# Performance work log

Measured on AMD Instinct MI355X. Metric: run time of the kernel, lower is better.

Reference implementation:

```python
import jax, jax.numpy as jnp
import numpy as np

N_WIRES = 10
DIM = 1 << N_WIRES  # 1024
EPS = 1e-12

_CNOT = jnp.array([[1, 0, 0, 0],
                   [0, 1, 0, 0],
                   [0, 0, 0, 1],
                   [0, 0, 1, 0]], dtype=jnp.complex64)

# signs[i, j] = (-1)^{bit_j(i)} for single-Z Pauli string on wire j (qubit 0 = MSB)
_bits = (np.arange(DIM)[:, None] >> (N_WIRES - 1 - np.arange(N_WIRES))[None, :]) & 1
_Z_SIGNS = jnp.asarray(1.0 - 2.0 * _bits, dtype=jnp.float32)  # (DIM, N_WIRES)


def _rx_gate(theta):
    c = jnp.cos(theta / 2).astype(jnp.complex64)
    s = jnp.sin(theta / 2).astype(jnp.complex64)
    return jnp.stack([jnp.stack([c, -1j * s]), jnp.stack([-1j * s, c])])


def _ry_gate(theta):
    c = jnp.cos(theta / 2).astype(jnp.complex64)
    s = jnp.sin(theta / 2).astype(jnp.complex64)
    return jnp.stack([jnp.stack([c, -s]), jnp.stack([s, c])])


def _apply_1q(psi, gate, q):
    # psi: (N, DIM) complex64; apply 2x2 gate on qubit q (qubit 0 = MSB)
    N = psi.shape[0]
    left, right = 1 << q, 1 << (N_WIRES - 1 - q)
    psi = psi.reshape(N, left, 2, right)
    psi = jnp.einsum('ab,nxby->nxay', gate, psi)
    return psi.reshape(N, DIM)


def _apply_2q(psi, gate, q0, q1):
    # gate: (4,4) acting on qubits (q0, q1) in that order
    G = gate.reshape(2, 2, 2, 2)
    if q0 > q1:
        G = jnp.transpose(G, (1, 0, 3, 2))
        q0, q1 = q1, q0
    N = psi.shape[0]
    a = 1 << q0
    b = 1 << (q1 - q0 - 1)
    c = 1 << (N_WIRES - 1 - q1)
    psi = psi.reshape(N, a, 2, b, 2, c)
    psi = jnp.einsum('ijkl,nxkylz->nxiyjz', G, psi)
    return psi.reshape(N, DIM)


def setup_inputs() -> dict:
    key = jax.random.key(0)
    k1, k2, k3, k4 = jax.random.split(key, 4)
    x = jax.random.normal(k1, (4, 1024, DIM), dtype=jnp.float32)
    rx0 = jax.random.normal(k2, (N_WIRES,), dtype=jnp.float32)
    ry0 = jax.random.normal(k3, (N_WIRES,), dtype=jnp.float32)
    ry1 = jax.random.normal(k4, (N_WIRES,), dtype=jnp.float32)
    return {"x": x, "rx0": rx0, "ry0": ry0, "ry1": ry1}


def reference(x, rx0, ry0, ry1):
    B, T, C = x.shape
    x_flat = x.reshape(B * T, C)
    # amplitude encoding: L2-normalize each row into a complex state vector
    norm = jnp.linalg.norm(x_flat, axis=1, keepdims=True)
    psi = (x_flat / jnp.maximum(norm, EPS)).astype(jnp.complex64)  # (N, DIM)
    # layer 1: RX then RY on each wire
    for j in range(N_WIRES):
        psi = _apply_1q(psi, _rx_gate(rx0[j]), j)
        psi = _apply_1q(psi, _ry_gate(ry0[j]), j)
    # CNOT ring
    for j in range(N_WIRES):
        psi = _apply_2q(psi, _CNOT, j, (j + 1) % N_WIRES)
    # layer 2: RY on each wire
    for j in range(N_WIRES):
        psi = _apply_1q(psi, _ry_gate(ry1[j]), j)
    # expectation values of Z on each wire: sum_i |psi_i|^2 * (-1)^{bit_j(i)}
    probs = psi.real ** 2 + psi.imag ** 2  # (N, DIM) float32
    out = probs @ _Z_SIGNS                  # (N, N_WIRES)
    return out.reshape(B, T, N_WIRES).astype(jnp.float32)
```

## Files before the change

### kernel.cpp

```cpp
#include <hip/hip_runtime.h>

#define NW 10

__device__ __forceinline__ int gperm(int v) {
    #pragma unroll
    for (int k = 9; k >= 0; --k) {
        const int cs = 9 - k;
        const int ts = 9 - ((k + 1) % NW);
        v ^= ((v >> cs) & 1) << ts;
    }
    return v;
}

__device__ __forceinline__ int PF(int i) {
    return i + ((i >> 5) << 2) + ((i >> 8) << 3);
}
#define PBUF 1176

template<int SH>
__device__ __forceinline__ void cg(float* re, float* im,
                                   float ar, float ai, float br, float bi) {
    #pragma unroll
    for (int base = 0; base < 16; base += (2 << SH)) {
        #pragma unroll
        for (int off = 0; off < (1 << SH); ++off) {
            const int r0 = base + off, r1 = r0 + (1 << SH);
            const float v0r = re[r0], v0i = im[r0];
            const float v1r = re[r1], v1i = im[r1];
            re[r0] =  ar * v0r - ai * v0i + br * v1r - bi * v1i;
            im[r0] =  ar * v0i + ai * v0r + br * v1i + bi * v1r;
            re[r1] = -br * v0r - bi * v0i + ar * v1r + ai * v1i;
            im[r1] =  bi * v0r - br * v0i + ar * v1i - ai * v1r;
        }
    }
}

template<int SH>
__device__ __forceinline__ void rg(float* re, float* im, float c, float s) {
    #pragma unroll
    for (int base = 0; base < 16; base += (2 << SH)) {
        #pragma unroll
        for (int off = 0; off < (1 << SH); ++off) {
            const int r0 = base + off, r1 = r0 + (1 << SH);
            const float v0r = re[r0], v0i = im[r0];
            const float v1r = re[r1], v1i = im[r1];
            re[r0] = c * v0r - s * v1r;  im[r0] = c * v0i - s * v1i;
            re[r1] = s * v0r + c * v1r;  im[r1] = s * v0i + c * v1i;
        }
    }
}

__global__ __launch_bounds__(64) void qsa_main(
    const float* __restrict__ x,
    const float* __restrict__ rx0,
    const float* __restrict__ ry0,
    const float* __restrict__ ry1,
    float* __restrict__ out) {

    __shared__ __align__(16) float reb[PBUF];
    __shared__ __align__(16) float imb[PBUF];
    __shared__ float cf[64];

    const int t = threadIdx.x;
    const int n = blockIdx.x;

    if (t < NW) {
        float sx, cx, sy0, cy0, sy1, cy1;
        sincosf(0.5f * rx0[t], &sx,  &cx);
        sincosf(0.5f * ry0[t], &sy0, &cy0);
        sincosf(0.5f * ry1[t], &sy1, &cy1);
        cf[4 * t + 0] =  cy0 * cx;
        cf[4 * t + 1] =  sy0 * sx;
        cf[4 * t + 2] = -sy0 * cx;
        cf[4 * t + 3] = -cy0 * sx;
        cf[40 + 2 * t]     = cy1;
        cf[40 + 2 * t + 1] = sy1;
    }

    float re[16], im[16];
    const float* xr = x + ((size_t)n << 10) + (t << 4);
    float ss = 0.f;
    #pragma unroll
    for (int r = 0; r < 16; r += 4) {
        const float4 v = *reinterpret_cast<const float4*>(xr + r);
        re[r] = v.x; re[r + 1] = v.y; re[r + 2] = v.z; re[r + 3] = v.w;
        ss += v.x * v.x + v.y * v.y + v.z * v.z + v.w * v.w;
    }
    #pragma unroll
    for (int b = 32; b > 0; b >>= 1) ss += __shfl_xor(ss, b, 64);
    const float scale = 1.0f / fmaxf(sqrtf(ss), 1e-12f);

    __syncthreads();

    {
        const float ar = cf[36], ai = cf[37], br = cf[38], bi = cf[39];
        #pragma unroll
        for (int r = 0; r < 16; r += 2) {
            const float v0 = re[r] * scale, v1 = re[r + 1] * scale;
            re[r]     =  ar * v0 + br * v1;  im[r]     = ai * v0 + bi * v1;
            re[r + 1] = -br * v0 + ar * v1;  im[r + 1] = bi * v0 - ai * v1;
        }
    }
    cg<1>(re, im, cf[32], cf[33], cf[34], cf[35]);
    cg<2>(re, im, cf[28], cf[29], cf[30], cf[31]);
    cg<3>(re, im, cf[24], cf[25], cf[26], cf[27]);

    #pragma unroll
    for (int r = 0; r < 16; r += 4) {
        const int p = PF((t << 4) + r);
        *reinterpret_cast<float4*>(&reb[p]) = make_float4(re[r], re[r+1], re[r+2], re[r+3]);
        *reinterpret_cast<float4*>(&imb[p]) = make_float4(im[r], im[r+1], im[r+2], im[r+3]);
    }
    __syncthreads();
    {
        const int b0 = ((t >> 4) << 8) | (t & 15);
        #pragma unroll
        for (int r = 0; r < 16; ++r) {
            const int p = PF(b0 + (r << 4));
            re[r] = reb[p]; im[r] = imb[p];
        }
    }

    cg<0>(re, im, cf[20], cf[21], cf[22], cf[23]);
    cg<1>(re, im, cf[16], cf[17], cf[18], cf[19]);
    cg<2>(re, im, cf[12], cf[13], cf[14], cf[15]);
    cg<3>(re, im, cf[ 8], cf[ 9], cf[10], cf[11]);

    {
        const int b0 = ((t >> 4) << 8) | (t & 15);
        #pragma unroll
        for (int r = 0; r < 16; ++r) {
            const int p = PF(b0 + (r << 4));
            reb[p] = re[r]; imb[p] = im[r];
        }
    }
    __syncthreads();
    #pragma unroll
    for (int r = 0; r < 16; r += 4) {
        const int p = PF(((r >> 2) << 8) | (t << 2));
        float4 q = *reinterpret_cast<const float4*>(&reb[p]);
        re[r] = q.x; re[r+1] = q.y; re[r+2] = q.z; re[r+3] = q.w;
        q = *reinterpret_cast<const float4*>(&imb[p]);
        im[r] = q.x; im[r+1] = q.y; im[r+2] = q.z; im[r+3] = q.w;
    }

    cg<2>(re, im, cf[4], cf[5], cf[6], cf[7]);
    cg<3>(re, im, cf[0], cf[1], cf[2], cf[3]);

    #pragma unroll
    for (int r = 0; r < 16; r += 4) {
        const int p = PF(((r >> 2) << 8) | (t << 2));
        *reinterpret_cast<float4*>(&reb[p]) = make_float4(re[r], re[r+1], re[r+2], re[r+3]);
        *reinterpret_cast<float4*>(&imb[p]) = make_float4(im[r], im[r+1], im[r+2], im[r+3]);
    }
    __syncthreads();
    {
        const int gt = gperm(t << 4);
        #pragma unroll
        for (int r = 0; r < 16; ++r) {
            const int p = PF(gt ^ gperm(r));
            re[r] = reb[p]; im[r] = imb[p];
        }
    }

    rg<0>(re, im, cf[58], cf[59]);
    rg<1>(re, im, cf[56], cf[57]);
    rg<2>(re, im, cf[54], cf[55]);
    rg<3>(re, im, cf[52], cf[53]);

    #pragma unroll
    for (int r = 0; r < 16; r += 4) {
        const int p = PF((t << 4) + r);
        *reinterpret_cast<float4*>(&reb[p]) = make_float4(re[r], re[r+1], re[r+2], re[r+3]);
        *reinterpret_cast<float4*>(&imb[p]) = make_float4(im[r], im[r+1], im[r+2], im[r+3]);
    }
    __syncthreads();
    {
        const int b0 = ((t >> 4) << 8) | (t & 15);
        #pragma unroll
        for (int r = 0; r < 16; ++r) {
            const int p = PF(b0 + (r << 4));
            re[r] = reb[p]; im[r] = imb[p];
        }
    }

    rg<0>(re, im, cf[50], cf[51]);
    rg<1>(re, im, cf[48], cf[49]);
    rg<2>(re, im, cf[46], cf[47]);
    rg<3>(re, im, cf[44], cf[45]);

    {
        const int b0 = ((t >> 4) << 8) | (t & 15);
        #pragma unroll
        for (int r = 0; r < 16; ++r) {
            const int p = PF(b0 + (r << 4));
            reb[p] = re[r]; imb[p] = im[r];
        }
    }
    __syncthreads();
    #pragma unroll
    for (int r = 0; r < 16; r += 4) {
        const int p = PF(((r >> 2) << 8) | (t << 2));
        float4 q = *reinterpret_cast<const float4*>(&reb[p]);
        re[r] = q.x; re[r+1] = q.y; re[r+2] = q.z; re[r+3] = q.w;
        q = *reinterpret_cast<const float4*>(&imb[p]);
        im[r] = q.x; im[r+1] = q.y; im[r+2] = q.z; im[r+3] = q.w;
    }

    rg<2>(re, im, cf[42], cf[43]);
    rg<3>(re, im, cf[40], cf[41]);

    float P = 0.f, a0 = 0.f, a1 = 0.f, a8 = 0.f, a9 = 0.f;
    #pragma unroll
    for (int r = 0; r < 16; ++r) {
        const float p = re[r] * re[r] + im[r] * im[r];
        P  += p;
        a0 += (r & 8) ? -p : p;
        a1 += (r & 4) ? -p : p;
        a8 += (r & 2) ? -p : p;
        a9 += (r & 1) ? -p : p;
    }
    #pragma unroll
    for (int b = 1; b < 64; b <<= 1) {
        a0 += __shfl_xor(a0, b, 64);
        a1 += __shfl_xor(a1, b, 64);
        a8 += __shfl_xor(a8, b, 64);
        a9 += __shfl_xor(a9, b, 64);
        const float e = __shfl_xor(P, b, 64);
        P = (t & b) ? (e - P) : (e + P);
    }
    float* o = out + (size_t)n * NW;
    if (t == 0) { o[0] = a0; o[1] = a1; o[8] = a8; o[9] = a9; }
    if (t == 32) o[2] = P;
    if (t == 16) o[3] = P;
    if (t ==  8) o[4] = P;
    if (t ==  4) o[5] = P;
    if (t ==  2) o[6] = P;
    if (t ==  1) o[7] = P;
}

extern "C" void kernel_launch(void* const* d_in, const int* in_sizes, int n_in,
                              void* d_out, int out_size, void* d_ws, size_t ws_size,
                              hipStream_t stream) {
    const float* x   = (const float*)d_in[0];
    const float* rx0 = (const float*)d_in[1];
    const float* ry0 = (const float*)d_in[2];
    const float* ry1 = (const float*)d_in[3];
    float* out = (float*)d_out;
    const int nstates = in_sizes[0] >> 10;
    qsa_main<<<nstates, 64, 0, stream>>>(x, rx0, ry0, ry1, out);
}
```

Before: 82.35 us.

## Interleave complex LDS layout, packed float2 math, readlane gate coefficients

Real and imaginary parts now live interleaved in one float2 shared buffer with a new padding function. That halves the number of separate LDS transactions per exchange and allows float4/float2 accesses. Gate coefficients are computed in lanes 0-9 and broadcast with readlane instead of going through a shared-memory table, which removes one barrier and the LDS reads. Gate arithmetic is written on 2-wide vectors so the compiler can emit packed FP32 instructions. The cost is possible bank conflicts from the new padding and higher register pressure.

Result: no change. 82.13 us (-0.3%).

```diff
diff --git a/kernel.cpp b/kernel.cpp
--- a/kernel.cpp
+++ b/kernel.cpp
@@ -1,6 +1,7 @@
 #include <hip/hip_runtime.h>
 
 #define NW 10
+typedef float f32x2 __attribute__((ext_vector_type(2)));
 
 __device__ __forceinline__ int gperm(int v) {
     #pragma unroll
@@ -12,41 +13,70 @@
     return v;
 }
 
-__device__ __forceinline__ int PF(int i) {
-    return i + ((i >> 5) << 2) + ((i >> 8) << 3);
-}
-#define PBUF 1176
+__device__ __forceinline__ int PQ(int i) {
+    return i + ((i >> 4) << 1) + ((i >> 8) << 1);
+}
+#define PBUF 1156
+
+__device__ __forceinline__ float rl(float v, int lane) {
+    return __int_as_float(__builtin_amdgcn_readlane(__float_as_int(v), lane));
+}
 
 template<int SH>
-__device__ __forceinline__ void cg(float* re, float* im,
-                                   float ar, float ai, float br, float bi) {
+__device__ __forceinline__ void cgp(float* re, float* im,
+                                    float ar, float ai, float br, float bi) {
     #pragma unroll
     for (int base = 0; base < 16; base += (2 << SH)) {
         #pragma unroll
-        for (int off = 0; off < (1 << SH); ++off) {
+        for (int off = 0; off < (1 << SH); off += 2) {
             const int r0 = base + off, r1 = r0 + (1 << SH);
-            const float v0r = re[r0], v0i = im[r0];
-            const float v1r = re[r1], v1i = im[r1];
-            re[r0] =  ar * v0r - ai * v0i + br * v1r - bi * v1i;
-            im[r0] =  ar * v0i + ai * v0r + br * v1i + bi * v1r;
-            re[r1] = -br * v0r - bi * v0i + ar * v1r + ai * v1i;
-            im[r1] =  bi * v0r - br * v0i + ar * v1i - ai * v1r;
-        }
+            const f32x2 v0r = {re[r0], re[r0+1]}, v0i = {im[r0], im[r0+1]};
+            const f32x2 v1r = {re[r1], re[r1+1]}, v1i = {im[r1], im[r1+1]};
+            const f32x2 n0r = ar*v0r - ai*v0i + br*v1r - bi*v1i;
+            const f32x2 n0i = ar*v0i + ai*v0r + br*v1i + bi*v1r;
+            const f32x2 n1r = ar*v1r + ai*v1i - br*v0r - bi*v0i;
+            const f32x2 n1i = ar*v1i - ai*v1r - br*v0i + bi*v0r;
+            re[r0]=n0r.x; re[r0+1]=n0r.y; im[r0]=n0i.x; im[r0+1]=n0i.y;
+            re[r1]=n1r.x; re[r1+1]=n1r.y; im[r1]=n1i.x; im[r1+1]=n1i.y;
+        }
+    }
+}
+
+__device__ __forceinline__ void cg0(float* re, float* im,
+                                    float ar, float ai, float br, float bi) {
+    #pragma unroll
+    for (int r = 0; r < 16; r += 2) {
+        const float v0r = re[r], v0i = im[r], v1r = re[r+1], v1i = im[r+1];
+        re[r]   =  ar*v0r - ai*v0i + br*v1r - bi*v1i;
+        im[r]   =  ar*v0i + ai*v0r + br*v1i + bi*v1r;
+        re[r+1] = -br*v0r - bi*v0i + ar*v1r + ai*v1i;
+        im[r+1] =  bi*v0r - br*v0i + ar*v1i - ai*v1r;
     }
 }
 
 template<int SH>
-__device__ __forceinline__ void rg(float* re, float* im, float c, float s) {
+__device__ __forceinline__ void rgp(float* re, float* im, float c, float s) {
     #pragma unroll
     for (int base = 0; base < 16; base += (2 << SH)) {
         #pragma unroll
-        for (int off = 0; off < (1 << SH); ++off) {
+        for (int off = 0; off < (1 << SH); off += 2) {
             const int r0 = base + off, r1 = r0 + (1 << SH);
-            const float v0r = re[r0], v0i = im[r0];
-            const float v1r = re[r1], v1i = im[r1];
-            re[r0] = c * v0r - s * v1r;  im[r0] = c * v0i - s * v1i;
-            re[r1] = s * v0r + c * v1r;  im[r1] = s * v0i + c * v1i;
-        }
+            const f32x2 v0r = {re[r0], re[r0+1]}, v0i = {im[r0], im[r0+1]};
+            const f32x2 v1r = {re[r1], re[r1+1]}, v1i = {im[r1], im[r1+1]};
+            const f32x2 n0r = c*v0r - s*v1r, n0i = c*v0i - s*v1i;
+            const f32x2 n1r = s*v0r + c*v1r, n1i = s*v0i + c*v1i;
+            re[r0]=n0r.x; re[r0+1]=n0r.y; im[r0]=n0i.x; im[r0+1]=n0i.y;
+            re[r1]=n1r.x; re[r1+1]=n1r.y; im[r1]=n1i.x; im[r1+1]=n1i.y;
+        }
+    }
+}
+
+__device__ __forceinline__ void rg0(float* re, float* im, float c, float s) {
+    #pragma unroll
+    for (int r = 0; r < 16; r += 2) {
+        const float v0r = re[r], v0i = im[r], v1r = re[r+1], v1i = im[r+1];
+        re[r]   = c*v0r - s*v1r;  im[r]   = c*v0i - s*v1i;
+        re[r+1] = s*v0r + c*v1r;  im[r+1] = s*v0i + c*v1i;
     }
 }
 
@@ -57,158 +87,144 @@
     const float* __restrict__ ry1,
     float* __restrict__ out) {
 
-    __shared__ __align__(16) float reb[PBUF];
-    __shared__ __align__(16) float imb[PBUF];
-    __shared__ float cf[64];
+    __shared__ __align__(16) float2 sp[PBUF];
 
     const int t = threadIdx.x;
     const int n = blockIdx.x;
 
+    float re[16], im[16];
+    const float* xr = x + ((size_t)n << 10) + (t << 4);
+    #pragma unroll
+    for (int r = 0; r < 16; r += 4) {
+        const float4 v = *reinterpret_cast<const float4*>(xr + r);
+        re[r] = v.x; re[r+1] = v.y; re[r+2] = v.z; re[r+3] = v.w;
+    }
+
+    float car = 0.f, cai = 0.f, cbr = 0.f, cbi = 0.f, cc1 = 0.f, cs1 = 0.f;
     if (t < NW) {
-        float sx, cx, sy0, cy0, sy1, cy1;
+        float sx, cx, sy0, cy0;
         sincosf(0.5f * rx0[t], &sx,  &cx);
         sincosf(0.5f * ry0[t], &sy0, &cy0);
-        sincosf(0.5f * ry1[t], &sy1, &cy1);
-        cf[4 * t + 0] =  cy0 * cx;
-        cf[4 * t + 1] =  sy0 * sx;
-        cf[4 * t + 2] = -sy0 * cx;
-        cf[4 * t + 3] = -cy0 * sx;
-        cf[40 + 2 * t]     = cy1;
-        cf[40 + 2 * t + 1] = sy1;
-    }
-
-    float re[16], im[16];
-    const float* xr = x + ((size_t)n << 10) + (t << 4);
+        sincosf(0.5f * ry1[t], &cs1, &cc1);
+        car =  cy0 * cx;  cai =  sy0 * sx;
+        cbr = -sy0 * cx;  cbi = -cy0 * sx;
+    }
+
     float ss = 0.f;
     #pragma unroll
-    for (int r = 0; r < 16; r += 4) {
-        const float4 v = *reinterpret_cast<const float4*>(xr + r);
-        re[r] = v.x; re[r + 1] = v.y; re[r + 2] = v.z; re[r + 3] = v.w;
-        ss += v.x * v.x + v.y * v.y + v.z * v.z + v.w * v.w;
-    }
+    for (int r = 0; r < 16; ++r) ss += re[r] * re[r];
     #pragma unroll
     for (int b = 32; b > 0; b >>= 1) ss += __shfl_xor(ss, b, 64);
     const float scale = 1.0f / fmaxf(sqrtf(ss), 1e-12f);
 
-    __syncthreads();
-
-    {
-        const float ar = cf[36], ai = cf[37], br = cf[38], bi = cf[39];
-        #pragma unroll
-        for (int r = 0; r < 16; r += 2) {
-            const float v0 = re[r] * scale, v1 = re[r + 1] * scale;
-            re[r]     =  ar * v0 + br * v1;  im[r]     = ai * v0 + bi * v1;
-            re[r + 1] = -br * v0 + ar * v1;  im[r + 1] = bi * v0 - ai * v1;
-        }
-    }
-    cg<1>(re, im, cf[32], cf[33], cf[34], cf[35]);
-    cg<2>(re, im, cf[28], cf[29], cf[30], cf[31]);
-    cg<3>(re, im, cf[24], cf[25], cf[26], cf[27]);
-
-    #pragma unroll
-    for (int r = 0; r < 16; r += 4) {
-        const int p = PF((t << 4) + r);
-        *reinterpret_cast<float4*>(&reb[p]) = make_float4(re[r], re[r+1], re[r+2], re[r+3]);
-        *reinterpret_cast<float4*>(&imb[p]) = make_float4(im[r], im[r+1], im[r+2], im[r+3]);
-    }
+    {
+        const float ar = rl(car,9), ai = rl(cai,9), br = rl(cbr,9), bi = rl(cbi,9);
+        #pragma unroll
+        for (int r = 0; r < 16; r += 4) {
+            const f32x2 v0 = {re[r] * scale,   re[r+2] * scale};
+            const f32x2 v1 = {re[r+1] * scale, re[r+3] * scale};
+            const f32x2 n0r = ar*v0 + br*v1, n0i = ai*v0 + bi*v1;
+            const f32x2 n1r = ar*v1 - br*v0, n1i = bi*v0 - ai*v1;
+            re[r]   = n0r.x; im[r]   = n0i.x; re[r+1] = n1r.x; im[r+1] = n1i.x;
+            re[r+2] = n0r.y; im[r+2] = n0i.y; re[r+3] = n1r.y; im[r+3] = n1i.y;
+        }
+    }
+    cgp<1>(re, im, rl(car,8), rl(cai,8), rl(cbr,8), rl(cbi,8));
+    cgp<2>(re, im, rl(car,7), rl(cai,7), rl(cbr,7), rl(cbi,7));
+    cgp<3>(re, im, rl(car,6), rl(cai,6), rl(cbr,6), rl(cbi,6));
+
+    #pragma unroll
+    for (int r = 0; r < 16; r += 2)
+        *reinterpret_cast<float4*>(&sp[PQ((t << 4) | r)]) =
+            make_float4(re[r], im[r], re[r+1], im[r+1]);
     __syncthreads();
     {
         const int b0 = ((t >> 4) << 8) | (t & 15);
         #pragma unroll
         for (int r = 0; r < 16; ++r) {
-            const int p = PF(b0 + (r << 4));
-            re[r] = reb[p]; im[r] = imb[p];
-        }
-    }
-
-    cg<0>(re, im, cf[20], cf[21], cf[22], cf[23]);
-    cg<1>(re, im, cf[16], cf[17], cf[18], cf[19]);
-    cg<2>(re, im, cf[12], cf[13], cf[14], cf[15]);
-    cg<3>(re, im, cf[ 8], cf[ 9], cf[10], cf[11]);
-
-    {
-        const int b0 = ((t >> 4) << 8) | (t & 15);
+            const float2 v = sp[PQ(b0 + (r << 4))];
+            re[r] = v.x; im[r] = v.y;
+        }
+    }
+
+    cg0   (re, im, rl(car,5), rl(cai,5), rl(cbr,5), rl(cbi,5));
+    cgp<1>(re, im, rl(car,4), rl(cai,4), rl(cbr,4), rl(cbi,4));
+    cgp<2>(re, im, rl(car,3), rl(cai,3), rl(cbr,3), rl(cbi,3));
+    cgp<3>(re, im, rl(car,2), rl(cai,2), rl(cbr,2), rl(cbi,2));
+
+    {
+        const int b0 = ((t >> 4) << 8) | (t & 15);
+        #pragma unroll
+        for (int r = 0; r < 16; ++r)
+            sp[PQ(b0 + (r << 4))] = make_float2(re[r], im[r]);
+    }
+    __syncthreads();
+    #pragma unroll
+    for (int r = 0; r < 16; r += 2) {
+        const int i = ((r >> 2) << 8) | (t << 2) | (r & 3);
+        const float4 q = *reinterpret_cast<const float4*>(&sp[PQ(i)]);
+        re[r] = q.x; im[r] = q.y; re[r+1] = q.z; im[r+1] = q.w;
+    }
+
+    cgp<2>(re, im, rl(car,1), rl(cai,1), rl(cbr,1), rl(cbi,1));
+    cgp<3>(re, im, rl(car,0), rl(cai,0), rl(cbr,0), rl(cbi,0));
+
+    #pragma unroll
+    for (int r = 0; r < 16; r += 2) {
+        const int i = ((r >> 2) << 8) | (t << 2) | (r & 3);
+        *reinterpret_cast<float4*>(&sp[PQ(i)]) =
+            make_float4(re[r], im[r], re[r+1], im[r+1]);
+    }
+    __syncthreads();
+    {
+        const int gt = gperm(t << 4);
         #pragma unroll
         for (int r = 0; r < 16; ++r) {
-            const int p = PF(b0 + (r << 4));
-            reb[p] = re[r]; imb[p] = im[r];
-        }
-    }
-    __syncthreads();
-    #pragma unroll
-    for (int r = 0; r < 16; r += 4) {
-        const int p = PF(((r >> 2) << 8) | (t << 2));
-        float4 q = *reinterpret_cast<const float4*>(&reb[p]);
-        re[r] = q.x; re[r+1] = q.y; re[r+2] = q.z; re[r+3] = q.w;
-        q = *reinterpret_cast<const float4*>(&imb[p]);
-        im[r] = q.x; im[r+1] = q.y; im[r+2] = q.z; im[r+3] = q.w;
-    }
-
-    cg<2>(re, im, cf[4], cf[5], cf[6], cf[7]);
-    cg<3>(re, im, cf[0], cf[1], cf[2], cf[3]);
-
-    #pragma unroll
-    for (int r = 0; r < 16; r += 4) {
-        const int p = PF(((r >> 2) << 8) | (t << 2));
-        *reinterpret_cast<float4*>(&reb[p]) = make_float4(re[r], re[r+1], re[r+2], re[r+3]);
-        *reinterpret_cast<float4*>(&imb[p]) = make_float4(im[r], im[r+1], im[r+2], im[r+3]);
-    }
-    __syncthreads();
-    {
-        const int gt = gperm(t << 4);
+            const float2 v = sp[PQ(gt ^ gperm(r))];
+            re[r] = v.x; im[r] = v.y;
+        }
+    }
+
+    rg0   (re, im, rl(cc1,9), rl(cs1,9));
+    rgp<1>(re, im, rl(cc1,8), rl(cs1,8));
+    rgp<2>(re, im, rl(cc1,7), rl(cs1,7));
+    rgp<3>(re, im, rl(cc1,6), rl(cs1,6));
+
+    #pragma unroll
+    for (int r = 0; r < 16; r += 2)
+        *reinterpret_cast<float4*>(&sp[PQ((t << 4) | r)]) =
+            make_float4(re[r], im[r], re[r+1], im[r+1]);
+    __syncthreads();
+    {
+        const int b0 = ((t >> 4) << 8) | (t & 15);
         #pragma unroll
         for (int r = 0; r < 16; ++r) {
-            const int p = PF(gt ^ gperm(r));
-            re[r] = reb[p]; im[r] = imb[p];
-        }
-    }
-
-    rg<0>(re, im, cf[58], cf[59]);
-    rg<1>(re, im, cf[56], cf[57]);
-    rg<2>(re, im, cf[54], cf[55]);
-    rg<3>(re, im, cf[52], cf[53]);
-
-    #pragma unroll
-    for (int r = 0; r < 16; r += 4) {
-        const int p = PF((t << 4) + r);
-        *reinterpret_cast<float4*>(&reb[p]) = make_float4(re[r], re[r+1], re[r+2], re[r+3]);
-        *reinterpret_cast<float4*>(&imb[p]) = make_float4(im[r], im[r+1], im[r+2], im[r+3]);
-    }
-    __syncthreads();
-    {
-        const int b0 = ((t >> 4) << 8) | (t & 15);
-        #pragma unroll
-        for (int r = 0; r < 16; ++r) {
-            const int p = PF(b0 + (r << 4));
-            re[r] = reb[p]; im[r] = imb[p];
-        }
-    }
-
-    rg<0>(re, im, cf[50], cf[51]);
-    rg<1>(re, im, cf[48], cf[49]);
-    rg<2>(re, im, cf[46], cf[47]);
-    rg<3>(re, im, cf[44], cf[45]);
-
-    {
-        const int b0 = ((t >> 4) << 8) | (t & 15);
-        #pragma unroll
-        for (int r = 0; r < 16; ++r) {
-            const int p = PF(b0 + (r << 4));
-            reb[p] = re[r]; imb[p] = im[r];
-        }
-    }
-    __syncthreads();
-    #pragma unroll
-    for (int r = 0; r < 16; r += 4) {
-        const int p = PF(((r >> 2) << 8) | (t << 2));
-        float4 q = *reinterpret_cast<const float4*>(&reb[p]);
-        re[r] = q.x; re[r+1] = q.y; re[r+2] = q.z; re[r+3] = q.w;
-        q = *reinterpret_cast<const float4*>(&imb[p]);
-        im[r] = q.x; im[r+1] = q.y; im[r+2] = q.z; im[r+3] = q.w;
-    }
-
-    rg<2>(re, im, cf[42], cf[43]);
-    rg<3>(re, im, cf[40], cf[41]);
+            const float2 v = sp[PQ(b0 + (r << 4))];
+            re[r] = v.x; im[r] = v.y;
+        }
+    }
+
+    rg0   (re, im, rl(cc1,5), rl(cs1,5));
+    rgp<1>(re, im, rl(cc1,4), rl(cs1,4));
+    rgp<2>(re, im, rl(cc1,3), rl(cs1,3));
+    rgp<3>(re, im, rl(cc1,2), rl(cs1,2));
+
+    {
+        const int b0 = ((t >> 4) << 8) | (t & 15);
+        #pragma unroll
+        for (int r = 0; r < 16; ++r)
+            sp[PQ(b0 + (r << 4))] = make_float2(re[r], im[r]);
+    }
+    __syncthreads();
+    #pragma unroll
+    for (int r = 0; r < 16; r += 2) {
+        const int i = ((r >> 2) << 8) | (t << 2) | (r & 3);
+        const float4 q = *reinterpret_cast<const float4*>(&sp[PQ(i)]);
+        re[r] = q.x; im[r] = q.y; re[r+1] = q.z; im[r+1] = q.w;
+    }
+
+    rgp<2>(re, im, rl(cc1,1), rl(cs1,1));
+    rgp<3>(re, im, rl(cc1,0), rl(cs1,0));
 
     float P = 0.f, a0 = 0.f, a1 = 0.f, a8 = 0.f, a9 = 0.f;
     #pragma unroll
```
